# Kernel tuning notes

Measured on AMD Instinct MI355X. Metric: run time of the kernel, lower is better.

The kernel has to match this reference:

```python
import jax, jax.numpy as jnp
import numpy as np


def setup_inputs() -> dict:
    key = jax.random.key(0)
    k1, k2, k3, k4 = jax.random.split(key, 4)
    B, D, H, W, N = 32, 16, 256, 256, 512
    pred_batch = jax.random.normal(k1, (B, D, H, W), dtype=jnp.float32)
    kpt_batch = jax.random.uniform(k2, (B, N, 2), dtype=jnp.float32)  # normalized coords in [0,1)
    vis_batch = jax.random.randint(k3, (B, N), 0, 2, dtype=jnp.int32)
    tag_batch = jax.random.randint(k4, (B, N), 0, 32, dtype=jnp.int32)
    return {"pred_batch": pred_batch, "kpt_batch": kpt_batch,
            "vis_batch": vis_batch, "tag_batch": tag_batch}


def reference(pred_batch, kpt_batch, vis_batch, tag_batch):
    B, D, H, W = pred_batch.shape
    dt = pred_batch.dtype
    # unnorm with [W, H] then floor to integer pixel indices (as in original)
    unnorm = jnp.array([W, H], dtype=dt)
    idx = jnp.floor(kpt_batch * unnorm).astype(jnp.int32)   # [B, N, 2]
    y, x = idx[..., 0], idx[..., 1]
    # gather embeddings at keypoint locations: [B, D, N]
    pred_ebd = jax.vmap(lambda p, yy, xx: p[:, yy, xx])(pred_batch, y, x)
    # visibility mask replaces the variable-length boolean selection
    mask = (vis_batch > 0).astype(dt)                       # [B, N]
    pair_mask = mask[:, :, None] * mask[:, None, :]         # [B, N, N]
    true_sim = (tag_batch[:, :, None] == tag_batch[:, None, :]).astype(dt)
    # exponent = mean_d (a_d - b_d)^2 = mean(a^2) + mean(b^2) - 2/D * a.b
    sq = jnp.mean(pred_ebd ** 2, axis=1)                    # [B, N]
    dot = jnp.einsum('bdn,bdm->bnm', pred_ebd, pred_ebd) / D
    exponent = sq[:, :, None] + sq[:, None, :] - 2.0 * dot  # [B, N, N]
    pred_sim = 2.0 / (1.0 + jnp.exp(exponent))
    wgt = jnp.where((true_sim > 0) | (pred_sim > 0), jnp.asarray(10.0, dt), jnp.asarray(0.0, dt))
    dis = (pred_sim - true_sim) ** 2
    K = jnp.sum(mask, axis=1)                               # visible count per sample
    denom = jnp.maximum(K * K, 1.0)
    per_sample = jnp.sum(dis * wgt * pair_mask, axis=(1, 2)) / denom
    return jnp.mean(per_sample)
```

## Files before the change

### kernel.cpp

```cpp
#include <hip/hip_runtime.h>
#include <math.h>

#define B_ 32
#define D_ 16
#define H_ 256
#define W_ 256
#define N_ 512
#define TS 64
#define NT 8
#define NPAIR 36
#define RS 20

__global__ __launch_bounds__(256) void tagloss_k(const float* __restrict__ pred,
                                                 const float* __restrict__ kpt,
                                                 const int* __restrict__ vis,
                                                 const int* __restrict__ tag,
                                                 float* __restrict__ out) {
    __shared__ float eA[TS * RS];
    __shared__ float eB[TS * RS];
    __shared__ float sqA[TS], sqB[TS];
    __shared__ int   tgA[TS], tgB[TS];
    __shared__ float msA[TS], msB[TS];
    __shared__ float redA[4], redK[4];

    int bi = blockIdx.x;
    int b  = bi / NPAIR;
    int p  = bi - b * NPAIR;
    int ti = 0, rem = p;
    while (rem >= (NT - ti)) { rem -= (NT - ti); ++ti; }
    int tj = ti + rem;

    int t = threadIdx.x;

    {
        int r    = t >> 1;
        int half = t & 1;
        int inA  = (r < TS);
        int rr   = inA ? r : (r - TS);
        int n    = (inA ? ti : tj) * TS + rr;
        float k0 = kpt[(b * N_ + n) * 2 + 0];
        float k1 = kpt[(b * N_ + n) * 2 + 1];
        int y = (int)floorf(k0 * (float)W_);
        int x = (int)floorf(k1 * (float)H_);
        y = min(max(y, 0), H_ - 1);
        x = min(max(x, 0), W_ - 1);
        const float* pb = pred + (((size_t)b * D_ + half * 8) * H_ + y) * W_ + x;
        float v[8];
#pragma unroll
        for (int dd = 0; dd < 8; ++dd) v[dd] = pb[(size_t)dd * (H_ * W_)];
        float psum = 0.f;
#pragma unroll
        for (int dd = 0; dd < 8; ++dd) psum += v[dd] * v[dd];
        float other = __shfl_xor(psum, 1);
        float sqm = (psum + other) * (1.0f / (float)D_);

        float* dst = (inA ? eA : eB) + rr * RS + half * 8;
        ((float4*)dst)[0] = make_float4(v[0], v[1], v[2], v[3]);
        ((float4*)dst)[1] = make_float4(v[4], v[5], v[6], v[7]);
        if (half == 0) {
            int   tgv = tag[b * N_ + n];
            float msv = (vis[b * N_ + n] > 0) ? 1.0f : 0.0f;
            if (inA) { sqA[rr] = sqm; tgA[rr] = tgv; msA[rr] = msv; }
            else     { sqB[rr] = sqm; tgB[rr] = tgv; msB[rr] = msv; }
        }
    }
    float kpart = ((vis[b * N_ + t] > 0) ? 1.0f : 0.0f) +
                  ((vis[b * N_ + t + 256] > 0) ? 1.0f : 0.0f);
    __syncthreads();

    int r2 = t >> 2;
    int q  = t & 3;
    const float4* ap = (const float4*)&eA[r2 * RS];
    float4 a0 = ap[0], a1 = ap[1], a2 = ap[2], a3 = ap[3];
    float sa = sqA[r2];
    int   tn = tgA[r2];
    float mn = msA[r2];

    float acc = 0.0f;
#pragma unroll 4
    for (int i = 0; i < 16; ++i) {
        int m = (i << 2) | q;
        const float4* bp = (const float4*)&eB[m * RS];
        float4 b0 = bp[0], b1 = bp[1], b2 = bp[2], b3 = bp[3];
        float dot;
        dot  = a0.x * b0.x; dot += a0.y * b0.y; dot += a0.z * b0.z; dot += a0.w * b0.w;
        dot += a1.x * b1.x; dot += a1.y * b1.y; dot += a1.z * b1.z; dot += a1.w * b1.w;
        dot += a2.x * b2.x; dot += a2.y * b2.y; dot += a2.z * b2.z; dot += a2.w * b2.w;
        dot += a3.x * b3.x; dot += a3.y * b3.y; dot += a3.z * b3.z; dot += a3.w * b3.w;
        float ex = sa + sqB[m] - 0.125f * dot;
        float ps = 2.0f / (1.0f + __expf(ex));
        float ts = (tn == tgB[m]) ? 1.0f : 0.0f;
        float di = ps - ts;
        acc += di * di * msB[m];
    }
    acc *= mn;

#pragma unroll
    for (int off = 32; off; off >>= 1) {
        acc   += __shfl_down(acc, off);
        kpart += __shfl_down(kpart, off);
    }
    if ((t & 63) == 0) { redA[t >> 6] = acc; redK[t >> 6] = kpart; }
    __syncthreads();
    if (t == 0) {
        float tot = redA[0] + redA[1] + redA[2] + redA[3];
        float K   = redK[0] + redK[1] + redK[2] + redK[3];
        float tilew = (ti == tj) ? 1.0f : 2.0f;
        float scale = 10.0f * tilew / (fmaxf(K * K, 1.0f) * (float)B_);
        atomicAdd(out, tot * scale);
    }
}

extern "C" void kernel_launch(void* const* d_in, const int* in_sizes, int n_in,
                              void* d_out, int out_size, void* d_ws, size_t ws_size,
                              hipStream_t stream) {
    const float* pred = (const float*)d_in[0];
    const float* kpt  = (const float*)d_in[1];
    const int*   vis  = (const int*)d_in[2];
    const int*   tag  = (const int*)d_in[3];
    float* out = (float*)d_out;

    hipMemsetAsync(out, 0, sizeof(float) * out_size, stream);
    tagloss_k<<<B_ * NPAIR, 256, 0, stream>>>(pred, kpt, vis, tag, out);
}
```

Before: 202.4 us.

## Split keypoint embedding gather into a separate prepass kernel

Adds a gather kernel that reads each keypoint's 16-channel embedding from the prediction map once, computes its mean square, and stores both in a compact workspace. The pairwise loss kernel then loads contiguous float4 embeddings instead of redoing scattered gathers, since each tile was previously gathered up to 8 times across tile pairs. The cost is an extra kernel launch and a workspace round trip, and the gather kernel's accesses are still scattered, with one thread per channel.

```diff
diff --git a/kernel.cpp b/kernel.cpp
--- a/kernel.cpp
+++ b/kernel.cpp
@@ -11,8 +11,35 @@
 #define NPAIR 36
 #define RS 20
 
-__global__ __launch_bounds__(256) void tagloss_k(const float* __restrict__ pred,
-                                                 const float* __restrict__ kpt,
+__global__ __launch_bounds__(256) void gather_k(const float* __restrict__ pred,
+                                                const float* __restrict__ kpt,
+                                                float* __restrict__ emb,
+                                                float* __restrict__ sq) {
+    int gid = blockIdx.x * 256 + threadIdx.x;
+    int d   = gid & (D_ - 1);
+    int pt  = gid >> 4;
+    int b   = pt >> 9;
+
+    float k0 = kpt[pt * 2 + 0];
+    float k1 = kpt[pt * 2 + 1];
+    int y = (int)floorf(k0 * (float)W_);
+    int x = (int)floorf(k1 * (float)H_);
+    y = min(max(y, 0), H_ - 1);
+    x = min(max(x, 0), W_ - 1);
+
+    float v = pred[(((size_t)b * D_ + d) * H_ + y) * W_ + x];
+    emb[(size_t)pt * D_ + d] = v;
+
+    float s = v * v;
+    s += __shfl_xor(s, 1);
+    s += __shfl_xor(s, 2);
+    s += __shfl_xor(s, 4);
+    s += __shfl_xor(s, 8);
+    if (d == 0) sq[pt] = s * (1.0f / (float)D_);
+}
+
+__global__ __launch_bounds__(256) void tagloss_k(const float* __restrict__ emb,
+                                                 const float* __restrict__ sqg,
                                                  const int* __restrict__ vis,
                                                  const int* __restrict__ tag,
                                                  float* __restrict__ out) {
@@ -38,26 +65,14 @@
         int inA  = (r < TS);
         int rr   = inA ? r : (r - TS);
         int n    = (inA ? ti : tj) * TS + rr;
-        float k0 = kpt[(b * N_ + n) * 2 + 0];
-        float k1 = kpt[(b * N_ + n) * 2 + 1];
-        int y = (int)floorf(k0 * (float)W_);
-        int x = (int)floorf(k1 * (float)H_);
-        y = min(max(y, 0), H_ - 1);
-        x = min(max(x, 0), W_ - 1);
-        const float* pb = pred + (((size_t)b * D_ + half * 8) * H_ + y) * W_ + x;
-        float v[8];
-#pragma unroll
-        for (int dd = 0; dd < 8; ++dd) v[dd] = pb[(size_t)dd * (H_ * W_)];
-        float psum = 0.f;
-#pragma unroll
-        for (int dd = 0; dd < 8; ++dd) psum += v[dd] * v[dd];
-        float other = __shfl_xor(psum, 1);
-        float sqm = (psum + other) * (1.0f / (float)D_);
-
+        const float4* src = (const float4*)&emb[((size_t)(b * N_ + n)) * D_ + half * 8];
+        float4 v0 = src[0];
+        float4 v1 = src[1];
         float* dst = (inA ? eA : eB) + rr * RS + half * 8;
-        ((float4*)dst)[0] = make_float4(v[0], v[1], v[2], v[3]);
-        ((float4*)dst)[1] = make_float4(v[4], v[5], v[6], v[7]);
+        ((float4*)dst)[0] = v0;
+        ((float4*)dst)[1] = v1;
         if (half == 0) {
+            float sqm = sqg[b * N_ + n];
             int   tgv = tag[b * N_ + n];
             float msv = (vis[b * N_ + n] > 0) ? 1.0f : 0.0f;
             if (inA) { sqA[rr] = sqm; tgA[rr] = tgv; msA[rr] = msv; }
@@ -120,6 +135,10 @@
     const int*   tag  = (const int*)d_in[3];
     float* out = (float*)d_out;
 
+    float* emb = (float*)d_ws;
+    float* sq  = emb + (size_t)B_ * N_ * D_;
+
     hipMemsetAsync(out, 0, sizeof(float) * out_size, stream);
-    tagloss_k<<<B_ * NPAIR, 256, 0, stream>>>(pred, kpt, vis, tag, out);
+    gather_k<<<(B_ * N_ * D_) / 256, 256, 0, stream>>>(pred, kpt, emb, sq);
+    tagloss_k<<<B_ * NPAIR, 256, 0, stream>>>(emb, sq, vis, tag, out);
 }
```

After: 196.8 us. 1.03x faster.
